# Kernel tuning notes

Measured on AMD Instinct MI355X. Metric: run time of the kernel, lower is better.

## Reference

```python
import jax, jax.numpy as jnp
import numpy as np

B, T, D = 4, 2048, 1024
H = 16
HD = D // H  # 64


def setup_inputs() -> dict:
    key = jax.random.key(0)
    k1, k2, k3 = jax.random.split(key, 3)
    x = jax.random.normal(k1, (B, T, D), dtype=jnp.float32)
    w_qkv = jax.random.normal(k2, (D, 3 * D), dtype=jnp.float32) * (1.0 / np.sqrt(D))
    w_out = jax.random.normal(k3, (D, D), dtype=jnp.float32) * (1.0 / np.sqrt(D))
    return {"x": x, "w_qkv": w_qkv, "w_out": w_out}


def reference(x, w_qkv, w_out):
    b, t, c = x.shape
    qkv = x @ w_qkv  # [B,T,3D]
    q, k, v = jnp.split(qkv, 3, axis=-1)

    def heads(u):
        return u.reshape(b, t, H, HD).transpose(0, 2, 1, 3)  # [B,H,T,HD]

    q, k, v = heads(q), heads(k), heads(v)
    scale = 1.0 / np.sqrt(HD).astype(np.float32)
    attn = jnp.einsum('bhqd,bhkd->bhqk', q, k) * scale  # [B,H,T,T]
    causal = jnp.tril(jnp.ones((t, t), dtype=bool))
    attn = jnp.where(causal[None, None, :, :], attn, -jnp.inf)
    attn = jax.nn.softmax(attn, axis=-1)
    y = jnp.einsum('bhqk,bhkd->bhqd', attn, v)  # [B,H,T,HD]
    y = y.transpose(0, 2, 1, 3).reshape(b, t, c)
    return y @ w_out
```

## Files before the change

### kernel.cpp

```cpp
#include <hip/hip_runtime.h>
#include <hip/hip_bf16.h>
#include <stdint.h>

#define B_    4
#define T_    2048
#define D_    1024
#define H_    16
#define HD_   64
#define ROWS_ (B_ * T_)
#define NQKV_ (3 * D_)

typedef __attribute__((ext_vector_type(8))) short bf16x8;
typedef __attribute__((ext_vector_type(4))) float f32x4;

__device__ __forceinline__ unsigned short f2bf(float f) {
    union { float f; uint32_t u; } v; v.f = f;
    uint32_t u = v.u;
    return (unsigned short)((u + 0x7FFFu + ((u >> 16) & 1u)) >> 16);
}

__device__ __forceinline__ uint32_t pack2_rtz(float a, float b) {
    union { float f; uint32_t u; } x, y; x.f = a; y.f = b;
    return (x.u >> 16) | (y.u & 0xFFFF0000u);
}

__device__ __forceinline__ void glds16(const unsigned short* g, unsigned short* l) {
    __builtin_amdgcn_global_load_lds(
        (const __attribute__((address_space(1))) void*)g,
        (__attribute__((address_space(3))) void*)l, 16, 0, 0);
}

__global__ void cvt_bf16_kernel(const float* __restrict__ in,
                                unsigned short* __restrict__ out, int n8) {
    int i = blockIdx.x * blockDim.x + threadIdx.x;
    if (i >= n8) return;
    float4 a = ((const float4*)in)[2 * i];
    float4 b = ((const float4*)in)[2 * i + 1];
    union { bf16x8 v; unsigned short s[8]; } o;
    o.s[0] = f2bf(a.x); o.s[1] = f2bf(a.y); o.s[2] = f2bf(a.z); o.s[3] = f2bf(a.w);
    o.s[4] = f2bf(b.x); o.s[5] = f2bf(b.y); o.s[6] = f2bf(b.z); o.s[7] = f2bf(b.w);
    ((bf16x8*)out)[i] = o.v;
}

__global__ __launch_bounds__(256) void tcvt2_kernel(const float* __restrict__ wqkv,
                                                    const float* __restrict__ wout,
                                                    unsigned short* __restrict__ oqkv,
                                                    unsigned short* __restrict__ oout,
                                                    float scale) {
    __shared__ float tile[64 * 65];
    const int t = threadIdx.x;
    const bool second = blockIdx.x >= 48;
    const float* in = second ? wout : wqkv;
    unsigned short* out = second ? oout : oqkv;
    const int N = second ? 1024 : 3072;
    const int ncut = second ? 0 : 1024;
    const int n0 = (second ? (blockIdx.x - 48) : blockIdx.x) * 64;
    const int k0 = blockIdx.y * 64;
    const int K = 1024;
#pragma unroll
    for (int it = 0; it < 4; ++it) {
        int id = it * 256 + t;
        int r = id >> 4, c = (id & 15) * 4;
        float4 v = *(const float4*)&in[(size_t)(k0 + r) * N + n0 + c];
        tile[r * 65 + c + 0] = v.x; tile[r * 65 + c + 1] = v.y;
        tile[r * 65 + c + 2] = v.z; tile[r * 65 + c + 3] = v.w;
    }
    __syncthreads();
#pragma unroll
    for (int it = 0; it < 2; ++it) {
        int id = it * 256 + t;
        int n = id >> 3, kc = (id & 7) * 8;
        float sc = (n0 + n < ncut) ? scale : 1.0f;
        union { bf16x8 v; unsigned short s[8]; } o;
#pragma unroll
        for (int i = 0; i < 8; ++i) o.s[i] = f2bf(tile[(kc + i) * 65 + n] * sc);
        *(bf16x8*)&out[(size_t)(n0 + n) * K + k0 + kc] = o.v;
    }
}

template<int OUT_BF16, int VSPLIT>
__global__ __launch_bounds__(256) void gemm128_kernel(
    const unsigned short* __restrict__ A,
    const unsigned short* __restrict__ Bt,
    void* __restrict__ Cp, int M, int K, int ldC,
    unsigned short* __restrict__ vt)
{
    __shared__ __align__(16) unsigned short As[128 * 64];
    __shared__ __align__(16) unsigned short Bs[128 * 64];

    const int t = threadIdx.x, w = t >> 6, lane = t & 63;
    const int wm = w >> 1, wn = w & 1;
    const int lm = lane & 15, lq = lane >> 4;
    const int m0 = blockIdx.y * 128, n0 = blockIdx.x * 128;

    f32x4 acc[4][4];
#pragma unroll
    for (int i = 0; i < 4; i++)
#pragma unroll
        for (int j = 0; j < 4; j++) acc[i][j] = (f32x4){0.f, 0.f, 0.f, 0.f};

    const unsigned short* Ap[4];
    const unsigned short* Bp[4];
#pragma unroll
    for (int s = 0; s < 4; s++) {
        int id = s * 256 + t;
        int row = id >> 3, gch = (id & 7) ^ (row & 7);
        Ap[s] = A  + (size_t)(m0 + row) * K + gch * 8;
        Bp[s] = Bt + (size_t)(n0 + row) * K + gch * 8;
    }

    for (int k0 = 0; k0 < K; k0 += 64) {
        __syncthreads();
#pragma unroll
        for (int s = 0; s < 4; s++) glds16(Ap[s] + k0, &As[(s * 256 + t) * 8]);
#pragma unroll
        for (int s = 0; s < 4; s++) glds16(Bp[s] + k0, &Bs[(s * 256 + t) * 8]);
        __syncthreads();

#pragma unroll
        for (int kh = 0; kh < 2; kh++) {
            bf16x8 af[4], bfr[4];
#pragma unroll
            for (int mt = 0; mt < 4; mt++) {
                int row = wm * 64 + mt * 16 + lm;
                int sch = (kh * 4 + lq) ^ (lm & 7);
                af[mt] = *(const bf16x8*)&As[row * 64 + sch * 8];
            }
#pragma unroll
            for (int nt = 0; nt < 4; nt++) {
                int row = wn * 64 + nt * 16 + lm;
                int sch = (kh * 4 + lq) ^ (lm & 7);
                bfr[nt] = *(const bf16x8*)&Bs[row * 64 + sch * 8];
            }
#pragma unroll
            for (int mt = 0; mt < 4; mt++)
#pragma unroll
                for (int nt = 0; nt < 4; nt++)
                    acc[mt][nt] = __builtin_amdgcn_mfma_f32_16x16x32_bf16(
                        af[mt], bfr[nt], acc[mt][nt], 0, 0, 0);
        }
    }

    if (VSPLIT && n0 >= 2048) {
#pragma unroll
        for (int mt = 0; mt < 4; mt++)
#pragma unroll
            for (int nt = 0; nt < 4; nt++) {
                int row0 = m0 + wm * 64 + mt * 16 + lq * 4;
                int col  = n0 + wn * 64 + nt * 16 + lm - 2048;
                int bb = row0 >> 11, tt = row0 & 2047;
                size_t vi = ((size_t)((bb * 16 + (col >> 6)) * 64 + (col & 63))) * 2048 + tt;
                uint2 pk;
                pk.x = (uint32_t)f2bf(acc[mt][nt][0]) | ((uint32_t)f2bf(acc[mt][nt][1]) << 16);
                pk.y = (uint32_t)f2bf(acc[mt][nt][2]) | ((uint32_t)f2bf(acc[mt][nt][3]) << 16);
                *(uint2*)&vt[vi] = pk;
            }
        return;
    }
#pragma unroll
    for (int mt = 0; mt < 4; mt++)
#pragma unroll
        for (int nt = 0; nt < 4; nt++)
#pragma unroll
            for (int r = 0; r < 4; r++) {
                int row = m0 + wm * 64 + mt * 16 + lq * 4 + r;
                int col = n0 + wn * 64 + nt * 16 + lm;
                if (OUT_BF16)
                    ((unsigned short*)Cp)[(size_t)row * ldC + col] = f2bf(acc[mt][nt][r]);
                else
                    ((float*)Cp)[(size_t)row * ldC + col] = acc[mt][nt][r];
            }
}

__global__ __launch_bounds__(256) void attn4_kernel(
    const unsigned short* __restrict__ qk,
    const unsigned short* __restrict__ vt,
    unsigned short* __restrict__ y)
{
    __shared__ __align__(16) unsigned short Ks[64 * 72];
    __shared__ __align__(16) unsigned short Vs[64 * 72];
    __shared__ __align__(16) unsigned short Ps[4][32 * 72];

    const int bh = blockIdx.x, pair = blockIdx.y;
    const int b = bh >> 4, h = bh & 15;
    const int t = threadIdx.x, w = t >> 6, lane = t & 63;
    const int lm = lane & 15, lq = lane >> 4;
    unsigned short* psw = Ps[w];

    const int r0 = t >> 3,           c0 = (t & 7) * 8;
    const int r1 = (256 + t) >> 3,   c1 = (t & 7) * 8;
    const unsigned short* kgb = qk + (size_t)(b * T_) * 2048 + D_ + h * HD_;
    const unsigned short* vgb = vt + (size_t)(bh * 64) * 2048;

    const bf16x8 onesf = {0x3F80, 0x3F80, 0x3F80, 0x3F80,
                          0x3F80, 0x3F80, 0x3F80, 0x3F80};

    for (int which = 0; which < 2; ++which) {
        const int qt = which ? pair : (15 - pair);
        const int q0 = qt * 128, qw0 = q0 + w * 32;

        bf16x8 qf[2][2];
#pragma unroll
        for (int mt = 0; mt < 2; mt++)
#pragma unroll
            for (int kk = 0; kk < 2; kk++)
                qf[mt][kk] = *(const bf16x8*)
                    &qk[(size_t)(b * T_ + qw0 + mt * 16 + lm) * 2048 + h * HD_ + kk * 32 + lq * 8];

        f32x4 o[2][4], osum[2];
#pragma unroll
        for (int mt = 0; mt < 2; mt++) {
            osum[mt] = (f32x4){0.f, 0.f, 0.f, 0.f};
#pragma unroll
            for (int dt = 0; dt < 4; dt++) o[mt][dt] = (f32x4){0.f, 0.f, 0.f, 0.f};
        }

        const int kend = q0 + 128;

        bf16x8 ka = *(const bf16x8*)&kgb[(size_t)(0 + r0) * 2048 + c0];
        bf16x8 kb = *(const bf16x8*)&kgb[(size_t)(0 + r1) * 2048 + c1];
        bf16x8 va = *(const bf16x8*)&vgb[(size_t)r0 * 2048 + 0 + c0];
        bf16x8 vb = *(const bf16x8*)&vgb[(size_t)r1 * 2048 + 0 + c1];

        for (int kt = 0; kt < kend; kt += 64) {
            __syncthreads();
            *(bf16x8*)&Ks[r0 * 72 + c0] = ka;
            *(bf16x8*)&Ks[r1 * 72 + c1] = kb;
            *(bf16x8*)&Vs[r0 * 72 + c0] = va;
            *(bf16x8*)&Vs[r1 * 72 + c1] = vb;
            int ktn = (kt + 64 < kend) ? kt + 64 : kt;
            ka = *(const bf16x8*)&kgb[(size_t)(ktn + r0) * 2048 + c0];
            kb = *(const bf16x8*)&kgb[(size_t)(ktn + r1) * 2048 + c1];
            va = *(const bf16x8*)&vgb[(size_t)r0 * 2048 + ktn + c0];
            vb = *(const bf16x8*)&vgb[(size_t)r1 * 2048 + ktn + c1];
            __syncthreads();
            if (kt >= qw0 + 32) continue;

            f32x4 st[4][2];
#pragma unroll
            for (int nt = 0; nt < 4; nt++)
#pragma unroll
                for (int mt = 0; mt < 2; mt++) st[nt][mt] = (f32x4){0.f, 0.f, 0.f, 0.f};
#pragma unroll
            for (int nt = 0; nt < 4; nt++)
#pragma unroll
                for (int kk = 0; kk < 2; kk++) {
                    bf16x8 kf = *(const bf16x8*)&Ks[(nt * 16 + lm) * 72 + kk * 32 + lq * 8];
#pragma unroll
                    for (int mt = 0; mt < 2; mt++)
                        st[nt][mt] = __builtin_amdgcn_mfma_f32_16x16x32_bf16(
                            kf, qf[mt][kk], st[nt][mt], 0, 0, 0);
                }

            const bool diag = (kt + 64 > qw0);
#pragma unroll
            for (int mt = 0; mt < 2; mt++) {
                const int qi = qw0 + mt * 16 + lm;
#pragma unroll
                for (int nt = 0; nt < 4; nt++) {
                    float p[4];
                    if (diag) {
                        const int kj0 = kt + nt * 16 + lq * 4;
#pragma unroll
                        for (int r = 0; r < 4; r++)
                            p[r] = (kj0 + r <= qi)
                                 ? __builtin_amdgcn_exp2f(st[nt][mt][r]) : 0.f;
                    } else {
#pragma unroll
                        for (int r = 0; r < 4; r++)
                            p[r] = __builtin_amdgcn_exp2f(st[nt][mt][r]);
                    }
                    uint2 pk;
                    pk.x = pack2_rtz(p[0], p[1]);
                    pk.y = pack2_rtz(p[2], p[3]);
                    *(uint2*)&psw[(mt * 16 + lm) * 72 + nt * 16 + lq * 4] = pk;
                }
            }

#pragma unroll
            for (int kk = 0; kk < 2; kk++) {
                bf16x8 pf0 = *(const bf16x8*)&psw[(lm) * 72 + kk * 32 + lq * 8];
                bf16x8 pf1 = *(const bf16x8*)&psw[(16 + lm) * 72 + kk * 32 + lq * 8];
                osum[0] = __builtin_amdgcn_mfma_f32_16x16x32_bf16(pf0, onesf, osum[0], 0, 0, 0);
                osum[1] = __builtin_amdgcn_mfma_f32_16x16x32_bf16(pf1, onesf, osum[1], 0, 0, 0);
#pragma unroll
                for (int dt = 0; dt < 4; dt++) {
                    bf16x8 vf = *(const bf16x8*)&Vs[(dt * 16 + lm) * 72 + kk * 32 + lq * 8];
                    o[0][dt] = __builtin_amdgcn_mfma_f32_16x16x32_bf16(pf0, vf, o[0][dt], 0, 0, 0);
                    o[1][dt] = __builtin_amdgcn_mfma_f32_16x16x32_bf16(pf1, vf, o[1][dt], 0, 0, 0);
                }
            }
        }

#pragma unroll
        for (int mt = 0; mt < 2; mt++)
#pragma unroll
            for (int r = 0; r < 4; r++) {
                float rli = 1.f / osum[mt][r];
#pragma unroll
                for (int dt = 0; dt < 4; dt++)
                    y[(size_t)(b * T_ + qw0 + mt * 16 + lq * 4 + r) * D_ + h * HD_ + dt * 16 + lm]
                        = f2bf(o[mt][dt][r] * rli);
            }
    }
}

extern "C" void kernel_launch(void* const* d_in, const int* in_sizes, int n_in,
                              void* d_out, int out_size, void* d_ws, size_t ws_size,
                              hipStream_t stream) {
    const float* x    = (const float*)d_in[0];
    const float* wqkv = (const float*)d_in[1];
    const float* wout = (const float*)d_in[2];
    float* out = (float*)d_out;

    char* ws = (char*)d_ws;
    unsigned short* xb     = (unsigned short*)ws; ws += (size_t)ROWS_ * D_ * 2;
    unsigned short* wqkvbt = (unsigned short*)ws; ws += (size_t)D_ * NQKV_ * 2;
    unsigned short* woutbt = (unsigned short*)ws; ws += (size_t)D_ * D_ * 2;
    unsigned short* qkb    = (unsigned short*)ws; ws += (size_t)ROWS_ * 2048 * 2;
    unsigned short* vtb    = (unsigned short*)ws; ws += (size_t)ROWS_ * D_ * 2;
    unsigned short* yb     = (unsigned short*)ws;

    const float SC = 0.18033688011112042f;

    cvt_bf16_kernel<<<ROWS_ * D_ / 8 / 256, 256, 0, stream>>>(x, xb, ROWS_ * D_ / 8);
    tcvt2_kernel<<<dim3(64, 16), 256, 0, stream>>>(wqkv, wout, wqkvbt, woutbt, SC);

    gemm128_kernel<1, 1><<<dim3(NQKV_ / 128, ROWS_ / 128), 256, 0, stream>>>(
        xb, wqkvbt, qkb, ROWS_, D_, 2048, vtb);

    attn4_kernel<<<dim3(B_ * H_, 8), 256, 0, stream>>>(qkb, vtb, yb);

    gemm128_kernel<0, 0><<<dim3(D_ / 128, ROWS_ / 128), 256, 0, stream>>>(
        yb, woutbt, out, ROWS_, D_, D_, nullptr);
}
```

Before: 242.0 us.

## Shrink attention query tiles to 64 rows and load K/V via direct-to-LDS swizzled copies

The attention kernel now gives each block a 64-row query tile, with 16 rows per wave instead of 32. This doubles the grid to 1024 blocks, and launch bounds request 4 blocks per CU. K/V tiles are copied with a global-to-LDS helper (glds16) into an XOR-swizzled unpadded layout instead of register-staged prefetch. The goals are better occupancy and load balance and avoiding LDS bank conflicts. In exchange, each K/V tile is reloaded by twice as many blocks, and the register prefetch overlap is gone.

After: 255.1 us. 1.05x slower.

```diff
diff --git a/kernel.cpp b/kernel.cpp
--- a/kernel.cpp
+++ b/kernel.cpp
@@ -172,136 +172,116 @@
             }
 }
 
-__global__ __launch_bounds__(256) void attn4_kernel(
+__global__ __launch_bounds__(256, 4) void attn5_kernel(
     const unsigned short* __restrict__ qk,
     const unsigned short* __restrict__ vt,
     unsigned short* __restrict__ y)
 {
-    __shared__ __align__(16) unsigned short Ks[64 * 72];
-    __shared__ __align__(16) unsigned short Vs[64 * 72];
-    __shared__ __align__(16) unsigned short Ps[4][32 * 72];
-
-    const int bh = blockIdx.x, pair = blockIdx.y;
+    __shared__ __align__(16) unsigned short Ks[64 * 64];
+    __shared__ __align__(16) unsigned short Vs[64 * 64];
+    __shared__ __align__(16) unsigned short Ps[4][16 * 72];
+
+    const int pair = blockIdx.x, bh = blockIdx.y;
     const int b = bh >> 4, h = bh & 15;
     const int t = threadIdx.x, w = t >> 6, lane = t & 63;
     const int lm = lane & 15, lq = lane >> 4;
     unsigned short* psw = Ps[w];
 
-    const int r0 = t >> 3,           c0 = (t & 7) * 8;
-    const int r1 = (256 + t) >> 3,   c1 = (t & 7) * 8;
     const unsigned short* kgb = qk + (size_t)(b * T_) * 2048 + D_ + h * HD_;
     const unsigned short* vgb = vt + (size_t)(bh * 64) * 2048;
 
+    const int sr0 = t >> 3, sr1 = sr0 + 32;
+    const int xc0 = ((t & 7) ^ (sr0 & 7)) * 8;
+    const int xc1 = ((t & 7) ^ (sr1 & 7)) * 8;
+    const unsigned short* kp0 = kgb + (size_t)sr0 * 2048 + xc0;
+    const unsigned short* kp1 = kgb + (size_t)sr1 * 2048 + xc1;
+    const unsigned short* vp0 = vgb + (size_t)sr0 * 2048 + xc0;
+    const unsigned short* vp1 = vgb + (size_t)sr1 * 2048 + xc1;
+
     const bf16x8 onesf = {0x3F80, 0x3F80, 0x3F80, 0x3F80,
                           0x3F80, 0x3F80, 0x3F80, 0x3F80};
 
     for (int which = 0; which < 2; ++which) {
-        const int qt = which ? pair : (15 - pair);
-        const int q0 = qt * 128, qw0 = q0 + w * 32;
-
-        bf16x8 qf[2][2];
-#pragma unroll
-        for (int mt = 0; mt < 2; mt++)
-#pragma unroll
-            for (int kk = 0; kk < 2; kk++)
-                qf[mt][kk] = *(const bf16x8*)
-                    &qk[(size_t)(b * T_ + qw0 + mt * 16 + lm) * 2048 + h * HD_ + kk * 32 + lq * 8];
-
-        f32x4 o[2][4], osum[2];
-#pragma unroll
-        for (int mt = 0; mt < 2; mt++) {
-            osum[mt] = (f32x4){0.f, 0.f, 0.f, 0.f};
-#pragma unroll
-            for (int dt = 0; dt < 4; dt++) o[mt][dt] = (f32x4){0.f, 0.f, 0.f, 0.f};
-        }
-
-        const int kend = q0 + 128;
-
-        bf16x8 ka = *(const bf16x8*)&kgb[(size_t)(0 + r0) * 2048 + c0];
-        bf16x8 kb = *(const bf16x8*)&kgb[(size_t)(0 + r1) * 2048 + c1];
-        bf16x8 va = *(const bf16x8*)&vgb[(size_t)r0 * 2048 + 0 + c0];
-        bf16x8 vb = *(const bf16x8*)&vgb[(size_t)r1 * 2048 + 0 + c1];
-
+        const int qt = which ? pair : (31 - pair);
+        const int q0 = qt * 64, qw0 = q0 + w * 16;
+
+        bf16x8 qf[2];
+#pragma unroll
+        for (int kk = 0; kk < 2; kk++)
+            qf[kk] = *(const bf16x8*)
+                &qk[(size_t)(b * T_ + qw0 + lm) * 2048 + h * HD_ + kk * 32 + lq * 8];
+
+        f32x4 o[4], osum;
+        osum = (f32x4){0.f, 0.f, 0.f, 0.f};
+#pragma unroll
+        for (int dt = 0; dt < 4; dt++) o[dt] = (f32x4){0.f, 0.f, 0.f, 0.f};
+
+        const int kend = q0 + 64;
         for (int kt = 0; kt < kend; kt += 64) {
             __syncthreads();
-            *(bf16x8*)&Ks[r0 * 72 + c0] = ka;
-            *(bf16x8*)&Ks[r1 * 72 + c1] = kb;
-            *(bf16x8*)&Vs[r0 * 72 + c0] = va;
-            *(bf16x8*)&Vs[r1 * 72 + c1] = vb;
-            int ktn = (kt + 64 < kend) ? kt + 64 : kt;
-            ka = *(const bf16x8*)&kgb[(size_t)(ktn + r0) * 2048 + c0];
-            kb = *(const bf16x8*)&kgb[(size_t)(ktn + r1) * 2048 + c1];
-            va = *(const bf16x8*)&vgb[(size_t)r0 * 2048 + ktn + c0];
-            vb = *(const bf16x8*)&vgb[(size_t)r1 * 2048 + ktn + c1];
+            glds16(kp0 + (size_t)kt * 2048, &Ks[t * 8]);
+            glds16(kp1 + (size_t)kt * 2048, &Ks[(256 + t) * 8]);
+            glds16(vp0 + kt, &Vs[t * 8]);
+            glds16(vp1 + kt, &Vs[(256 + t) * 8]);
             __syncthreads();
-            if (kt >= qw0 + 32) continue;
-
-            f32x4 st[4][2];
+            if (kt >= qw0 + 16) continue;
+
+            f32x4 st[4];
+#pragma unroll
+            for (int nt = 0; nt < 4; nt++) st[nt] = (f32x4){0.f, 0.f, 0.f, 0.f};
 #pragma unroll
             for (int nt = 0; nt < 4; nt++)
 #pragma unroll
-                for (int mt = 0; mt < 2; mt++) st[nt][mt] = (f32x4){0.f, 0.f, 0.f, 0.f};
-#pragma unroll
-            for (int nt = 0; nt < 4; nt++)
-#pragma unroll
                 for (int kk = 0; kk < 2; kk++) {
-                    bf16x8 kf = *(const bf16x8*)&Ks[(nt * 16 + lm) * 72 + kk * 32 + lq * 8];
-#pragma unroll
-                    for (int mt = 0; mt < 2; mt++)
-                        st[nt][mt] = __builtin_amdgcn_mfma_f32_16x16x32_bf16(
-                            kf, qf[mt][kk], st[nt][mt], 0, 0, 0);
+                    bf16x8 kf = *(const bf16x8*)
+                        &Ks[(nt * 16 + lm) * 64 + ((kk * 4 + lq) ^ (lm & 7)) * 8];
+                    st[nt] = __builtin_amdgcn_mfma_f32_16x16x32_bf16(
+                        kf, qf[kk], st[nt], 0, 0, 0);
                 }
 
             const bool diag = (kt + 64 > qw0);
-#pragma unroll
-            for (int mt = 0; mt < 2; mt++) {
-                const int qi = qw0 + mt * 16 + lm;
-#pragma unroll
-                for (int nt = 0; nt < 4; nt++) {
-                    float p[4];
-                    if (diag) {
-                        const int kj0 = kt + nt * 16 + lq * 4;
-#pragma unroll
-                        for (int r = 0; r < 4; r++)
-                            p[r] = (kj0 + r <= qi)
-                                 ? __builtin_amdgcn_exp2f(st[nt][mt][r]) : 0.f;
-                    } else {
-#pragma unroll
-                        for (int r = 0; r < 4; r++)
-                            p[r] = __builtin_amdgcn_exp2f(st[nt][mt][r]);
-                    }
-                    uint2 pk;
-                    pk.x = pack2_rtz(p[0], p[1]);
-                    pk.y = pack2_rtz(p[2], p[3]);
-                    *(uint2*)&psw[(mt * 16 + lm) * 72 + nt * 16 + lq * 4] = pk;
+            const int qi = qw0 + lm;
+#pragma unroll
+            for (int nt = 0; nt < 4; nt++) {
+                float p[4];
+                if (diag) {
+                    const int kj0 = kt + nt * 16 + lq * 4;
+#pragma unroll
+                    for (int r = 0; r < 4; r++)
+                        p[r] = (kj0 + r <= qi)
+                             ? __builtin_amdgcn_exp2f(st[nt][r]) : 0.f;
+                } else {
+#pragma unroll
+                    for (int r = 0; r < 4; r++)
+                        p[r] = __builtin_amdgcn_exp2f(st[nt][r]);
                 }
+                uint2 pk;
+                pk.x = pack2_rtz(p[0], p[1]);
+                pk.y = pack2_rtz(p[2], p[3]);
+                *(uint2*)&psw[lm * 72 + nt * 16 + lq * 4] = pk;
             }
 
 #pragma unroll
             for (int kk = 0; kk < 2; kk++) {
-                bf16x8 pf0 = *(const bf16x8*)&psw[(lm) * 72 + kk * 32 + lq * 8];
-                bf16x8 pf1 = *(const bf16x8*)&psw[(16 + lm) * 72 + kk * 32 + lq * 8];
-                osum[0] = __builtin_amdgcn_mfma_f32_16x16x32_bf16(pf0, onesf, osum[0], 0, 0, 0);
-                osum[1] = __builtin_amdgcn_mfma_f32_16x16x32_bf16(pf1, onesf, osum[1], 0, 0, 0);
+                bf16x8 pf = *(const bf16x8*)&psw[lm * 72 + kk * 32 + lq * 8];
+                osum = __builtin_amdgcn_mfma_f32_16x16x32_bf16(pf, onesf, osum, 0, 0, 0);
 #pragma unroll
                 for (int dt = 0; dt < 4; dt++) {
-                    bf16x8 vf = *(const bf16x8*)&Vs[(dt * 16 + lm) * 72 + kk * 32 + lq * 8];
-                    o[0][dt] = __builtin_amdgcn_mfma_f32_16x16x32_bf16(pf0, vf, o[0][dt], 0, 0, 0);
-                    o[1][dt] = __builtin_amdgcn_mfma_f32_16x16x32_bf16(pf1, vf, o[1][dt], 0, 0, 0);
+                    bf16x8 vf = *(const bf16x8*)
+                        &Vs[(dt * 16 + lm) * 64 + ((kk * 4 + lq) ^ (lm & 7)) * 8];
+                    o[dt] = __builtin_amdgcn_mfma_f32_16x16x32_bf16(pf, vf, o[dt], 0, 0, 0);
                 }
             }
         }
 
 #pragma unroll
-        for (int mt = 0; mt < 2; mt++)
-#pragma unroll
-            for (int r = 0; r < 4; r++) {
-                float rli = 1.f / osum[mt][r];
-#pragma unroll
-                for (int dt = 0; dt < 4; dt++)
-                    y[(size_t)(b * T_ + qw0 + mt * 16 + lq * 4 + r) * D_ + h * HD_ + dt * 16 + lm]
-                        = f2bf(o[mt][dt][r] * rli);
-            }
+        for (int r = 0; r < 4; r++) {
+            float rli = 1.f / osum[r];
+#pragma unroll
+            for (int dt = 0; dt < 4; dt++)
+                y[(size_t)(b * T_ + qw0 + lq * 4 + r) * D_ + h * HD_ + dt * 16 + lm]
+                    = f2bf(o[dt][r] * rli);
+        }
     }
 }
 
@@ -329,7 +309,7 @@
     gemm128_kernel<1, 1><<<dim3(NQKV_ / 128, ROWS_ / 128), 256, 0, stream>>>(
         xb, wqkvbt, qkb, ROWS_, D_, 2048, vtb);
 
-    attn4_kernel<<<dim3(B_ * H_, 8), 256, 0, stream>>>(qkb, vtb, yb);
+    attn5_kernel<<<dim3(16, B_ * H_), 256, 0, stream>>>(qkb, vtb, yb);
 
     gemm128_kernel<0, 0><<<dim3(D_ / 128, ROWS_ / 128), 256, 0, stream>>>(
         yb, woutbt, out, ROWS_, D_, D_, nullptr);
```

## Split paired causal q-tiles into separate blocks and XOR-swizzle K/V LDS

Applied to the files above, without the earlier changes.

The attention kernel now launches one block per 128-row query tile (16 x 64 grid) instead of one block handling a paired heavy/light tile. The longest tiles are scheduled first via qt = 15 - blockIdx.x. K and V shared tiles drop their 72-element padding in favour of an XOR swizzle of 8-element chunks, which shrinks LDS use. The kernel also adds a min-blocks-per-CU hint of 4 to raise occupancy. In exchange, per-block work is less balanced and the Q loads and prologue are repeated across twice as many blocks.

Result: slower. 272.5 us (+12.6%).

```diff
diff --git a/kernel.cpp b/kernel.cpp
--- a/kernel.cpp
+++ b/kernel.cpp
@@ -172,137 +172,138 @@
             }
 }
 
-__global__ __launch_bounds__(256) void attn4_kernel(
+__global__ __launch_bounds__(256, 4) void attn6_kernel(
     const unsigned short* __restrict__ qk,
     const unsigned short* __restrict__ vt,
     unsigned short* __restrict__ y)
 {
-    __shared__ __align__(16) unsigned short Ks[64 * 72];
-    __shared__ __align__(16) unsigned short Vs[64 * 72];
+    __shared__ __align__(16) unsigned short Ks[64 * 64];
+    __shared__ __align__(16) unsigned short Vs[64 * 64];
     __shared__ __align__(16) unsigned short Ps[4][32 * 72];
 
-    const int bh = blockIdx.x, pair = blockIdx.y;
+    const int bh = blockIdx.y;
+    const int qt = 15 - blockIdx.x;
     const int b = bh >> 4, h = bh & 15;
     const int t = threadIdx.x, w = t >> 6, lane = t & 63;
     const int lm = lane & 15, lq = lane >> 4;
     unsigned short* psw = Ps[w];
 
-    const int r0 = t >> 3,           c0 = (t & 7) * 8;
-    const int r1 = (256 + t) >> 3,   c1 = (t & 7) * 8;
+    const int r0 = t >> 3, r1 = r0 + 32, gc = (t & 7) * 8;
+    const int xc0 = (((t & 7) ^ (r0 & 7))) * 8;
+    const int xc1 = (((t & 7) ^ (r1 & 7))) * 8;
     const unsigned short* kgb = qk + (size_t)(b * T_) * 2048 + D_ + h * HD_;
     const unsigned short* vgb = vt + (size_t)(bh * 64) * 2048;
 
     const bf16x8 onesf = {0x3F80, 0x3F80, 0x3F80, 0x3F80,
                           0x3F80, 0x3F80, 0x3F80, 0x3F80};
 
-    for (int which = 0; which < 2; ++which) {
-        const int qt = which ? pair : (15 - pair);
-        const int q0 = qt * 128, qw0 = q0 + w * 32;
-
-        bf16x8 qf[2][2];
-#pragma unroll
-        for (int mt = 0; mt < 2; mt++)
-#pragma unroll
-            for (int kk = 0; kk < 2; kk++)
-                qf[mt][kk] = *(const bf16x8*)
-                    &qk[(size_t)(b * T_ + qw0 + mt * 16 + lm) * 2048 + h * HD_ + kk * 32 + lq * 8];
-
-        f32x4 o[2][4], osum[2];
+    const int q0 = qt * 128, qw0 = q0 + w * 32;
+
+    bf16x8 qf[2][2];
+#pragma unroll
+    for (int mt = 0; mt < 2; mt++)
+#pragma unroll
+        for (int kk = 0; kk < 2; kk++)
+            qf[mt][kk] = *(const bf16x8*)
+                &qk[(size_t)(b * T_ + qw0 + mt * 16 + lm) * 2048 + h * HD_ + kk * 32 + lq * 8];
+
+    f32x4 o[2][4], osum[2];
+#pragma unroll
+    for (int mt = 0; mt < 2; mt++) {
+        osum[mt] = (f32x4){0.f, 0.f, 0.f, 0.f};
+#pragma unroll
+        for (int dt = 0; dt < 4; dt++) o[mt][dt] = (f32x4){0.f, 0.f, 0.f, 0.f};
+    }
+
+    const int kend = q0 + 128;
+
+    bf16x8 ka = *(const bf16x8*)&kgb[(size_t)r0 * 2048 + gc];
+    bf16x8 kb = *(const bf16x8*)&kgb[(size_t)r1 * 2048 + gc];
+    bf16x8 va = *(const bf16x8*)&vgb[(size_t)r0 * 2048 + gc];
+    bf16x8 vb = *(const bf16x8*)&vgb[(size_t)r1 * 2048 + gc];
+
+    for (int kt = 0; kt < kend; kt += 64) {
+        __syncthreads();
+        *(bf16x8*)&Ks[r0 * 64 + xc0] = ka;
+        *(bf16x8*)&Ks[r1 * 64 + xc1] = kb;
+        *(bf16x8*)&Vs[r0 * 64 + xc0] = va;
+        *(bf16x8*)&Vs[r1 * 64 + xc1] = vb;
+        int ktn = (kt + 64 < kend) ? kt + 64 : kt;
+        ka = *(const bf16x8*)&kgb[(size_t)(ktn + r0) * 2048 + gc];
+        kb = *(const bf16x8*)&kgb[(size_t)(ktn + r1) * 2048 + gc];
+        va = *(const bf16x8*)&vgb[(size_t)r0 * 2048 + ktn + gc];
+        vb = *(const bf16x8*)&vgb[(size_t)r1 * 2048 + ktn + gc];
+        __syncthreads();
+        if (kt >= qw0 + 32) continue;
+
+        f32x4 st[4][2];
+#pragma unroll
+        for (int nt = 0; nt < 4; nt++)
+#pragma unroll
+            for (int mt = 0; mt < 2; mt++) st[nt][mt] = (f32x4){0.f, 0.f, 0.f, 0.f};
+#pragma unroll
+        for (int nt = 0; nt < 4; nt++)
+#pragma unroll
+            for (int kk = 0; kk < 2; kk++) {
+                bf16x8 kf = *(const bf16x8*)
+                    &Ks[(nt * 16 + lm) * 64 + ((kk * 4 + lq) ^ (lm & 7)) * 8];
+#pragma unroll
+                for (int mt = 0; mt < 2; mt++)
+                    st[nt][mt] = __builtin_amdgcn_mfma_f32_16x16x32_bf16(
+                        kf, qf[mt][kk], st[nt][mt], 0, 0, 0);
+            }
+
+        const bool diag = (kt + 64 > qw0);
 #pragma unroll
         for (int mt = 0; mt < 2; mt++) {
-            osum[mt] = (f32x4){0.f, 0.f, 0.f, 0.f};
-#pragma unroll
-            for (int dt = 0; dt < 4; dt++) o[mt][dt] = (f32x4){0.f, 0.f, 0.f, 0.f};
+            const int qi = qw0 + mt * 16 + lm;
+#pragma unroll
+            for (int nt = 0; nt < 4; nt++) {
+                float p[4];
+                if (diag) {
+                    const int kj0 = kt + nt * 16 + lq * 4;
+#pragma unroll
+                    for (int r = 0; r < 4; r++)
+                        p[r] = (kj0 + r <= qi)
+                             ? __builtin_amdgcn_exp2f(st[nt][mt][r]) : 0.f;
+                } else {
+#pragma unroll
+                    for (int r = 0; r < 4; r++)
+                        p[r] = __builtin_amdgcn_exp2f(st[nt][mt][r]);
+                }
+                uint2 pk;
+                pk.x = pack2_rtz(p[0], p[1]);
+                pk.y = pack2_rtz(p[2], p[3]);
+                *(uint2*)&psw[(mt * 16 + lm) * 72 + nt * 16 + lq * 4] = pk;
+            }
         }
 
-        const int kend = q0 + 128;
-
-        bf16x8 ka = *(const bf16x8*)&kgb[(size_t)(0 + r0) * 2048 + c0];
-        bf16x8 kb = *(const bf16x8*)&kgb[(size_t)(0 + r1) * 2048 + c1];
-        bf16x8 va = *(const bf16x8*)&vgb[(size_t)r0 * 2048 + 0 + c0];
-        bf16x8 vb = *(const bf16x8*)&vgb[(size_t)r1 * 2048 + 0 + c1];
-
-        for (int kt = 0; kt < kend; kt += 64) {
-            __syncthreads();
-            *(bf16x8*)&Ks[r0 * 72 + c0] = ka;
-            *(bf16x8*)&Ks[r1 * 72 + c1] = kb;
-            *(bf16x8*)&Vs[r0 * 72 + c0] = va;
-            *(bf16x8*)&Vs[r1 * 72 + c1] = vb;
-            int ktn = (kt + 64 < kend) ? kt + 64 : kt;
-            ka = *(const bf16x8*)&kgb[(size_t)(ktn + r0) * 2048 + c0];
-            kb = *(const bf16x8*)&kgb[(size_t)(ktn + r1) * 2048 + c1];
-            va = *(const bf16x8*)&vgb[(size_t)r0 * 2048 + ktn + c0];
-            vb = *(const bf16x8*)&vgb[(size_t)r1 * 2048 + ktn + c1];
-            __syncthreads();
-            if (kt >= qw0 + 32) continue;
-
-            f32x4 st[4][2];
-#pragma unroll
-            for (int nt = 0; nt < 4; nt++)
-#pragma unroll
-                for (int mt = 0; mt < 2; mt++) st[nt][mt] = (f32x4){0.f, 0.f, 0.f, 0.f};
-#pragma unroll
-            for (int nt = 0; nt < 4; nt++)
-#pragma unroll
-                for (int kk = 0; kk < 2; kk++) {
-                    bf16x8 kf = *(const bf16x8*)&Ks[(nt * 16 + lm) * 72 + kk * 32 + lq * 8];
-#pragma unroll
-                    for (int mt = 0; mt < 2; mt++)
-                        st[nt][mt] = __builtin_amdgcn_mfma_f32_16x16x32_bf16(
-                            kf, qf[mt][kk], st[nt][mt], 0, 0, 0);
-                }
-
-            const bool diag = (kt + 64 > qw0);
-#pragma unroll
-            for (int mt = 0; mt < 2; mt++) {
-                const int qi = qw0 + mt * 16 + lm;
-#pragma unroll
-                for (int nt = 0; nt < 4; nt++) {
-                    float p[4];
-                    if (diag) {
-                        const int kj0 = kt + nt * 16 + lq * 4;
-#pragma unroll
-                        for (int r = 0; r < 4; r++)
-                            p[r] = (kj0 + r <= qi)
-                                 ? __builtin_amdgcn_exp2f(st[nt][mt][r]) : 0.f;
-                    } else {
-#pragma unroll
-                        for (int r = 0; r < 4; r++)
-                            p[r] = __builtin_amdgcn_exp2f(st[nt][mt][r]);
-                    }
-                    uint2 pk;
-                    pk.x = pack2_rtz(p[0], p[1]);
-                    pk.y = pack2_rtz(p[2], p[3]);
-                    *(uint2*)&psw[(mt * 16 + lm) * 72 + nt * 16 + lq * 4] = pk;
-                }
-            }
-
-#pragma unroll
-            for (int kk = 0; kk < 2; kk++) {
-                bf16x8 pf0 = *(const bf16x8*)&psw[(lm) * 72 + kk * 32 + lq * 8];
-                bf16x8 pf1 = *(const bf16x8*)&psw[(16 + lm) * 72 + kk * 32 + lq * 8];
-                osum[0] = __builtin_amdgcn_mfma_f32_16x16x32_bf16(pf0, onesf, osum[0], 0, 0, 0);
-                osum[1] = __builtin_amdgcn_mfma_f32_16x16x32_bf16(pf1, onesf, osum[1], 0, 0, 0);
-#pragma unroll
-                for (int dt = 0; dt < 4; dt++) {
-                    bf16x8 vf = *(const bf16x8*)&Vs[(dt * 16 + lm) * 72 + kk * 32 + lq * 8];
-                    o[0][dt] = __builtin_amdgcn_mfma_f32_16x16x32_bf16(pf0, vf, o[0][dt], 0, 0, 0);
-                    o[1][dt] = __builtin_amdgcn_mfma_f32_16x16x32_bf16(pf1, vf, o[1][dt], 0, 0, 0);
-                }
+#pragma unroll
+        for (int kk = 0; kk < 2; kk++) {
+            bf16x8 pf0 = *(const bf16x8*)&psw[(lm) * 72 + kk * 32 + lq * 8];
+            bf16x8 pf1 = *(const bf16x8*)&psw[(16 + lm) * 72 + kk * 32 + lq * 8];
+            osum[0] = __builtin_amdgcn_mfma_f32_16x16x32_bf16(pf0, onesf, osum[0], 0, 0, 0);
+            osum[1] = __builtin_amdgcn_mfma_f32_16x16x32_bf16(pf1, onesf, osum[1], 0, 0, 0);
+#pragma unroll
+            for (int dt = 0; dt < 4; dt++) {
+                bf16x8 vf = *(const bf16x8*)
+                    &Vs[(dt * 16 + lm) * 64 + ((kk * 4 + lq) ^ (lm & 7)) * 8];
+                o[0][dt] = __builtin_amdgcn_mfma_f32_16x16x32_bf16(pf0, vf, o[0][dt], 0, 0, 0);
+                o[1][dt] = __builtin_amdgcn_mfma_f32_16x16x32_bf16(pf1, vf, o[1][dt], 0, 0, 0);
             }
         }
-
-#pragma unroll
-        for (int mt = 0; mt < 2; mt++)
-#pragma unroll
-            for (int r = 0; r < 4; r++) {
-                float rli = 1.f / osum[mt][r];
-#pragma unroll
-                for (int dt = 0; dt < 4; dt++)
-                    y[(size_t)(b * T_ + qw0 + mt * 16 + lq * 4 + r) * D_ + h * HD_ + dt * 16 + lm]
-                        = f2bf(o[mt][dt][r] * rli);
-            }
-    }
+    }
+
+#pragma unroll
+    for (int mt = 0; mt < 2; mt++)
+#pragma unroll
+        for (int r = 0; r < 4; r++) {
+            float rli = 1.f / osum[mt][r];
+#pragma unroll
+            for (int dt = 0; dt < 4; dt++)
+                y[(size_t)(b * T_ + qw0 + mt * 16 + lq * 4 + r) * D_ + h * HD_ + dt * 16 + lm]
+                    = f2bf(o[mt][dt][r] * rli);
+        }
 }
 
 extern "C" void kernel_launch(void* const* d_in, const int* in_sizes, int n_in,
@@ -329,7 +330,7 @@
     gemm128_kernel<1, 1><<<dim3(NQKV_ / 128, ROWS_ / 128), 256, 0, stream>>>(
         xb, wqkvbt, qkb, ROWS_, D_, 2048, vtb);
 
-    attn4_kernel<<<dim3(B_ * H_, 8), 256, 0, stream>>>(qkb, vtb, yb);
+    attn6_kernel<<<dim3(16, B_ * H_), 256, 0, stream>>>(qkb, vtb, yb);
 
     gemm128_kernel<0, 0><<<dim3(D_ / 128, ROWS_ / 128), 256, 0, stream>>>(
         yb, woutbt, out, ROWS_, D_, D_, nullptr);
```
